# Kernel optimization log

Measured on AMD Instinct MI355X. Metric: run time of the kernel, lower is better.

Reference implementation:

```python
import jax, jax.numpy as jnp
import numpy as np

NEG = -1e6

def setup_inputs() -> dict:
    key = jax.random.key(0)
    ks = jax.random.split(key, 7)
    B, Q, K, H, Dv = 16, 64, 1024, 256, 256
    return {
        "queries": jax.random.normal(ks[0], (B, Q, H), jnp.float32),
        "keys": jax.random.normal(ks[1], (B, K, H), jnp.float32),
        "values": jax.random.normal(ks[2], (B, K, Dv), jnp.float32),
        "valid_lens": jax.random.randint(ks[3], (B,), 1, K + 1),
        "Wq": jax.random.normal(ks[4], (H, H), jnp.float32) / np.sqrt(H),
        "Wk": jax.random.normal(ks[5], (H, H), jnp.float32) / np.sqrt(H),
        "wv": jax.random.normal(ks[6], (H,), jnp.float32) / np.sqrt(H),
    }

def reference(queries, keys, values, valid_lens, Wq, Wk, wv):
    # projections: [B,Q,H], [B,K,H]
    q = jnp.einsum("bqd,hd->bqh", queries, Wq)
    k = jnp.einsum("bkd,hd->bkh", keys, Wk)
    # broadcast add + tanh: [B,Q,K,H]
    features = jnp.tanh(q[:, :, None, :] + k[:, None, :, :])
    # score reduction over hidden: [B,Q,K]
    scores = jnp.einsum("bqkh,h->bqk", features, wv)
    # masked softmax over the key axis (1D valid_lens per batch)
    K = keys.shape[1]
    mask = jnp.arange(K)[None, None, :] < valid_lens[:, None, None]  # [B,1,K]
    scores = jnp.where(mask, scores, NEG)
    attn = jax.nn.softmax(scores, axis=-1)
    # weighted sum over values: [B,Q,Dv]
    return jnp.einsum("bqk,bkv->bqv", attn, values)
```

## Files before the change

### kernel.cpp

```cpp
#include <hip/hip_runtime.h>

#define LOG2E 1.4426950408889634f
#define TANH_SCALE 2.8853900817779268f
#define NEG_BIG -1e30f

typedef __attribute__((ext_vector_type(8))) short bf16x8;
typedef __attribute__((ext_vector_type(4))) float f32x4;
typedef _Float16 half4 __attribute__((ext_vector_type(4)));

static __device__ __forceinline__ short f2bf(float f) {
    unsigned u = __builtin_bit_cast(unsigned, f);
    u += 0x7fffu + ((u >> 16) & 1u);
    return (short)(u >> 16);
}

__global__ __launch_bounds__(256) void proj_mfma(const float* __restrict__ queries,
                                                 const float* __restrict__ keys,
                                                 const float* __restrict__ Wq,
                                                 const float* __restrict__ Wk,
                                                 float* __restrict__ eq,
                                                 float* __restrict__ ek4) {
    const int mt = blockIdx.x >> 1, nt = blockIdx.x & 1;
    const int tid = threadIdx.x;
    const int w = tid >> 6, lane = tid & 63;
    const int wm = w >> 1, wn = w & 1;
    const int r = lane & 15, kq = lane >> 4;
    const int m0 = mt << 5;
    const int ncol = (nt << 7) + (wn << 6);

    const float* A; const float* W; int ar;
    if (m0 < 1024) { A = queries; W = Wq; ar = m0; }
    else           { A = keys;    W = Wk; ar = m0 - 1024; }

    const float* aptr = &A[(size_t)(ar + (wm << 4) + r) * 256];
    f32x4 acc[4] = {};

    #pragma unroll 2
    for (int ks = 0; ks < 8; ++ks) {
        const int k0 = (ks << 5) + (kq << 3);
        float4 fa0 = *reinterpret_cast<const float4*>(aptr + k0);
        float4 fa1 = *reinterpret_cast<const float4*>(aptr + k0 + 4);
        bf16x8 a = {f2bf(fa0.x), f2bf(fa0.y), f2bf(fa0.z), f2bf(fa0.w),
                    f2bf(fa1.x), f2bf(fa1.y), f2bf(fa1.z), f2bf(fa1.w)};
        #pragma unroll
        for (int nj = 0; nj < 4; ++nj) {
            const float* bp = &W[(size_t)(ncol + (nj << 4) + r) * 256 + k0];
            float4 fb0 = *reinterpret_cast<const float4*>(bp);
            float4 fb1 = *reinterpret_cast<const float4*>(bp + 4);
            bf16x8 bb = {f2bf(fb0.x), f2bf(fb0.y), f2bf(fb0.z), f2bf(fb0.w),
                         f2bf(fb1.x), f2bf(fb1.y), f2bf(fb1.z), f2bf(fb1.w)};
            acc[nj] = __builtin_amdgcn_mfma_f32_16x16x32_bf16(a, bb, acc[nj], 0, 0, 0);
        }
    }
    if (m0 < 1024) {
        #pragma unroll
        for (int nj = 0; nj < 4; ++nj)
            #pragma unroll
            for (int t = 0; t < 4; ++t) {
                int row = m0 + (wm << 4) + (kq << 2) + t;
                int col = ncol + (nj << 4) + r;
                eq[(size_t)row * 256 + col] =
                    __builtin_amdgcn_exp2f(TANH_SCALE * acc[nj][t]);
            }
    } else {
        #pragma unroll
        for (int nj = 0; nj < 4; ++nj)
            #pragma unroll
            for (int t = 0; t < 4; ++t) {
                int R   = (m0 - 1024) + (wm << 4) + (kq << 2) + t;
                int col = ncol + (nj << 4) + r;
                size_t idx = ((size_t)((col >> 2) << 14) + R) * 4 + (col & 3);
                ek4[idx] = __builtin_amdgcn_exp2f(TANH_SCALE * acc[nj][t]);
            }
    }
}

__global__ __launch_bounds__(256, 4) void attn_kernel(const float* __restrict__ eq,
                                                      const float* __restrict__ ek4,
                                                      const float* __restrict__ values,
                                                      const int* __restrict__ valid_lens,
                                                      const float* __restrict__ wv,
                                                      _Float16* __restrict__ part_acc,
                                                      float* __restrict__ part_m,
                                                      float* __restrict__ part_l) {
    __shared__ float4 q_lds[8 * 64];
    __shared__ float4 wv_lds[64];
    __shared__ float  p_lds[8][64];

    const int tid = threadIdx.x;
    const int w = tid >> 6, lane = tid & 63;

    const unsigned u = blockIdx.x;
    const int xcd = u & 7;
    const int j   = u >> 3;
    const int qt  = j & 7;
    const int pair = ((j >> 3) << 3) | xcd;
    const int b = pair & 15, seg = pair >> 4;

    const int q0 = qt << 3;
    const int vl = valid_lens[b];
    const int kstart = seg << 7;
    const int pA = (((b << 6) + q0 + (w << 1)) << 3) + seg;
    const int pB = pA + 8;

    if (kstart >= vl) {
        half4 z = {};
        *reinterpret_cast<half4*>(&part_acc[(size_t)pA * 256 + (lane << 2)]) = z;
        *reinterpret_cast<half4*>(&part_acc[(size_t)pB * 256 + (lane << 2)]) = z;
        if (lane == 0) {
            part_m[pA] = NEG_BIG; part_l[pA] = 0.f;
            part_m[pB] = NEG_BIG; part_l[pB] = 0.f;
        }
        return;
    }

    const float4* eqf = reinterpret_cast<const float4*>(eq);
    #pragma unroll
    for (int it = 0; it < 2; ++it) {
        int idx = tid + (it << 8);
        q_lds[idx] = eqf[(size_t)((b << 6) + q0 + (idx >> 6)) * 64 + (idx & 63)];
    }
    if (tid < 64) wv_lds[tid] = *(reinterpret_cast<const float4*>(wv) + tid);
    __syncthreads();

    const int kend = min(kstart + 128, vl);
    const int nchunks = (kend - kstart + 63) >> 6;

    const float4* ek4f = reinterpret_cast<const float4*>(ek4);
    const float4* qa4 = &q_lds[(w << 1) << 6];
    const float4* qb4 = qa4 + 64;

    float mA = -INFINITY, lA = 0.f, mB = -INFINITY, lB = 0.f;
    f32x4 accA = {0.f, 0.f, 0.f, 0.f}, accB = {0.f, 0.f, 0.f, 0.f};

    for (int c = 0; c < nchunks; ++c) {
        const int ck = kstart + (c << 6);
        const float4* ekc = ek4f + (size_t)((b << 10) + ck + lane);

        float sa0 = 0.f, sa1 = 0.f, sa2 = 0.f, sa3 = 0.f;
        float sb0 = 0.f, sb1 = 0.f, sb2 = 0.f, sb3 = 0.f;
        #pragma unroll 8
        for (int h4 = 0; h4 < 64; ++h4) {
            float4 ev = ekc[h4 << 14];
            float4 qa = qa4[h4];
            float4 qb = qb4[h4];
            float4 wc = wv_lds[h4];
            sa0 += wc.x * __builtin_amdgcn_rcpf(fmaf(ev.x, qa.x, 1.0f));
            sa1 += wc.y * __builtin_amdgcn_rcpf(fmaf(ev.y, qa.y, 1.0f));
            sa2 += wc.z * __builtin_amdgcn_rcpf(fmaf(ev.z, qa.z, 1.0f));
            sa3 += wc.w * __builtin_amdgcn_rcpf(fmaf(ev.w, qa.w, 1.0f));
            sb0 += wc.x * __builtin_amdgcn_rcpf(fmaf(ev.x, qb.x, 1.0f));
            sb1 += wc.y * __builtin_amdgcn_rcpf(fmaf(ev.y, qb.y, 1.0f));
            sb2 += wc.z * __builtin_amdgcn_rcpf(fmaf(ev.z, qb.z, 1.0f));
            sb3 += wc.w * __builtin_amdgcn_rcpf(fmaf(ev.w, qb.w, 1.0f));
        }
        float sA_ = -2.0f * ((sa0 + sa1) + (sa2 + sa3));
        float sB_ = -2.0f * ((sb0 + sb1) + (sb2 + sb3));
        if (ck + lane >= vl) { sA_ = NEG_BIG; sB_ = NEG_BIG; }

        float mcA = sA_, mcB = sB_;
        #pragma unroll
        for (int o = 32; o > 0; o >>= 1) {
            mcA = fmaxf(mcA, __shfl_xor(mcA, o));
            mcB = fmaxf(mcB, __shfl_xor(mcB, o));
        }
        float mnA = fmaxf(mA, mcA), mnB = fmaxf(mB, mcB);
        float rA = __builtin_amdgcn_exp2f((mA - mnA) * LOG2E);
        float rB = __builtin_amdgcn_exp2f((mB - mnB) * LOG2E);
        float pA_ = __builtin_amdgcn_exp2f((sA_ - mnA) * LOG2E);
        float pB_ = __builtin_amdgcn_exp2f((sB_ - mnB) * LOG2E);
        float lcA = pA_, lcB = pB_;
        #pragma unroll
        for (int o = 32; o > 0; o >>= 1) {
            lcA += __shfl_xor(lcA, o);
            lcB += __shfl_xor(lcB, o);
        }
        lA = lA * rA + lcA; mA = mnA;
        lB = lB * rB + lcB; mB = mnB;
        accA *= rA; accB *= rB;
        p_lds[(w << 1) + 0][lane] = pA_;
        p_lds[(w << 1) + 1][lane] = pB_;

        const int nv = min(64, kend - ck);
        const float* vsrc = &values[(size_t)(b * 1024 + ck) * 256 + (lane << 2)];
        if (nv == 64) {
            #pragma unroll 4
            for (int j4 = 0; j4 < 16; ++j4) {
                float4 pa4 = *reinterpret_cast<const float4*>(&p_lds[(w << 1)][j4 << 2]);
                float4 pb4 = *reinterpret_cast<const float4*>(&p_lds[(w << 1) + 1][j4 << 2]);
                #pragma unroll
                for (int jj = 0; jj < 4; ++jj) {
                    float pa = ((const float*)&pa4)[jj], pb = ((const float*)&pb4)[jj];
                    float4 v = *reinterpret_cast<const float4*>(vsrc + (((j4 << 2) + jj)) * 256);
                    accA.x += pa * v.x; accA.y += pa * v.y; accA.z += pa * v.z; accA.w += pa * v.w;
                    accB.x += pb * v.x; accB.y += pb * v.y; accB.z += pb * v.z; accB.w += pb * v.w;
                }
            }
        } else {
            for (int jx = 0; jx < nv; ++jx) {
                float pa = p_lds[(w << 1)][jx], pb = p_lds[(w << 1) + 1][jx];
                float4 v = *reinterpret_cast<const float4*>(vsrc + jx * 256);
                accA.x += pa * v.x; accA.y += pa * v.y; accA.z += pa * v.z; accA.w += pa * v.w;
                accB.x += pb * v.x; accB.y += pb * v.y; accB.z += pb * v.z; accB.w += pb * v.w;
            }
        }
    }

    if (lane == 0) {
        part_m[pA] = mA; part_l[pA] = lA;
        part_m[pB] = mB; part_l[pB] = lB;
    }
    half4 ha = {(_Float16)accA.x, (_Float16)accA.y, (_Float16)accA.z, (_Float16)accA.w};
    half4 hb = {(_Float16)accB.x, (_Float16)accB.y, (_Float16)accB.z, (_Float16)accB.w};
    *reinterpret_cast<half4*>(&part_acc[(size_t)pA * 256 + (lane << 2)]) = ha;
    *reinterpret_cast<half4*>(&part_acc[(size_t)pB * 256 + (lane << 2)]) = hb;
}

__global__ __launch_bounds__(256) void combine_kernel(const _Float16* __restrict__ part_acc,
                                                      const float* __restrict__ part_m,
                                                      const float* __restrict__ part_l,
                                                      float* __restrict__ out) {
    const int tid = threadIdx.x;
    const int w = tid >> 6, lane = tid & 63;
    const int b = blockIdx.x >> 4, qt = blockIdx.x & 15;
    const int q = (qt << 2) + w;
    const int base = ((b << 6) + q) << 3;

    float mm[8], ll[8];
    #pragma unroll
    for (int i = 0; i < 8; ++i) { mm[i] = part_m[base + i]; ll[i] = part_l[base + i]; }
    float M = mm[0];
    #pragma unroll
    for (int i = 1; i < 8; ++i) M = fmaxf(M, mm[i]);
    float wt[8];
    float L = 0.f;
    #pragma unroll
    for (int i = 0; i < 8; ++i) {
        wt[i] = __builtin_amdgcn_exp2f((mm[i] - M) * LOG2E);
        L += wt[i] * ll[i];
    }
    float invL = 1.0f / L;
    float4 o = {0.f, 0.f, 0.f, 0.f};
    #pragma unroll
    for (int i = 0; i < 8; ++i) {
        half4 v = *reinterpret_cast<const half4*>(&part_acc[(size_t)(base + i) * 256 + (lane << 2)]);
        o.x += wt[i] * (float)v.x; o.y += wt[i] * (float)v.y;
        o.z += wt[i] * (float)v.z; o.w += wt[i] * (float)v.w;
    }
    o.x *= invL; o.y *= invL; o.z *= invL; o.w *= invL;
    *reinterpret_cast<float4*>(&out[(size_t)((b << 6) + q) * 256 + (lane << 2)]) = o;
}

extern "C" void kernel_launch(void* const* d_in, const int* in_sizes, int n_in,
                              void* d_out, int out_size, void* d_ws, size_t ws_size,
                              hipStream_t stream) {
    const float* queries    = (const float*)d_in[0];
    const float* keys       = (const float*)d_in[1];
    const float* values     = (const float*)d_in[2];
    const int*   valid_lens = (const int*)d_in[3];
    const float* Wq         = (const float*)d_in[4];
    const float* Wk         = (const float*)d_in[5];
    const float* wv         = (const float*)d_in[6];
    float* out = (float*)d_out;

    float*     eq       = (float*)d_ws;
    float*     ek4      = eq + 262144;
    _Float16*  part_acc = (_Float16*)(ek4 + 4194304);
    float*     part_m   = (float*)(part_acc + 2097152);
    float*     part_l   = part_m + 8192;

    proj_mfma<<<dim3(1088), 256, 0, stream>>>(queries, keys, Wq, Wk, eq, ek4);
    attn_kernel<<<dim3(1024), 256, 0, stream>>>(eq, ek4, values, valid_lens, wv,
                                                part_acc, part_m, part_l);
    combine_kernel<<<dim3(256), 256, 0, stream>>>(part_acc, part_m, part_l, out);
}
```

Before: 193.4 us.

## Restructure attention: each wave scores 8 queries over its own 64-key chunk

```diff
diff --git a/kernel.cpp b/kernel.cpp
--- a/kernel.cpp
+++ b/kernel.cpp
@@ -20,6 +20,8 @@
                                                  const float* __restrict__ Wk,
                                                  float* __restrict__ eq,
                                                  float* __restrict__ ek4) {
+    __shared__ float lds_t[128][33];
+
     const int mt = blockIdx.x >> 1, nt = blockIdx.x & 1;
     const int tid = threadIdx.x;
     const int w = tid >> 6, lane = tid & 63;
@@ -67,11 +69,22 @@
         for (int nj = 0; nj < 4; ++nj)
             #pragma unroll
             for (int t = 0; t < 4; ++t) {
-                int R   = (m0 - 1024) + (wm << 4) + (kq << 2) + t;
-                int col = ncol + (nj << 4) + r;
-                size_t idx = ((size_t)((col >> 2) << 14) + R) * 4 + (col & 3);
-                ek4[idx] = __builtin_amdgcn_exp2f(TANH_SCALE * acc[nj][t]);
+                int rloc = (wm << 4) + (kq << 2) + t;
+                int hloc = (wn << 6) + (nj << 4) + r;
+                lds_t[hloc][rloc] = __builtin_amdgcn_exp2f(TANH_SCALE * acc[nj][t]);
             }
+        __syncthreads();
+        const int g0 = nt << 5;
+        const int R0 = m0 - 1024;
+        float4* ek4f = reinterpret_cast<float4*>(ek4);
+        #pragma unroll
+        for (int it = 0; it < 4; ++it) {
+            int idx = (it << 8) + tid;
+            int gl = idx >> 5, kk = idx & 31;
+            float4 v = {lds_t[(gl << 2) + 0][kk], lds_t[(gl << 2) + 1][kk],
+                        lds_t[(gl << 2) + 2][kk], lds_t[(gl << 2) + 3][kk]};
+            ek4f[((size_t)(g0 + gl) << 14) + R0 + kk] = v;
+        }
     }
 }
 
@@ -85,135 +98,97 @@
                                                       float* __restrict__ part_l) {
     __shared__ float4 q_lds[8 * 64];
     __shared__ float4 wv_lds[64];
-    __shared__ float  p_lds[8][64];
+    __shared__ float  p_lds[4][8][64];
 
     const int tid = threadIdx.x;
     const int w = tid >> 6, lane = tid & 63;
-
-    const unsigned u = blockIdx.x;
-    const int xcd = u & 7;
-    const int j   = u >> 3;
-    const int qt  = j & 7;
-    const int pair = ((j >> 3) << 3) | xcd;
-    const int b = pair & 15, seg = pair >> 4;
-
-    const int q0 = qt << 3;
+    const int qoct = blockIdx.x, b = blockIdx.y, seg = blockIdx.z;
+    const int q0 = qoct << 3;
     const int vl = valid_lens[b];
-    const int kstart = seg << 7;
-    const int pA = (((b << 6) + q0 + (w << 1)) << 3) + seg;
-    const int pB = pA + 8;
+    const int cidx = (seg << 2) + w;
+    const int kstart = cidx << 6;
+
+    const float4* eqf = reinterpret_cast<const float4*>(eq);
+    q_lds[tid]       = eqf[(size_t)((b << 6) + q0 + (tid >> 6)) * 64 + (tid & 63)];
+    q_lds[tid + 256] = eqf[(size_t)((b << 6) + q0 + (tid >> 6) + 4) * 64 + (tid & 63)];
+    if (tid < 64) wv_lds[tid] = reinterpret_cast<const float4*>(wv)[tid];
+    __syncthreads();
+
+    const int pbase = ((b << 6) + q0) << 4;
 
     if (kstart >= vl) {
         half4 z = {};
-        *reinterpret_cast<half4*>(&part_acc[(size_t)pA * 256 + (lane << 2)]) = z;
-        *reinterpret_cast<half4*>(&part_acc[(size_t)pB * 256 + (lane << 2)]) = z;
+        #pragma unroll
+        for (int qq = 0; qq < 8; ++qq)
+            *reinterpret_cast<half4*>(
+                &part_acc[(size_t)(pbase + (qq << 4) + cidx) * 256 + (lane << 2)]) = z;
+        if (lane < 8) {
+            part_m[pbase + (lane << 4) + cidx] = NEG_BIG;
+            part_l[pbase + (lane << 4) + cidx] = 0.f;
+        }
+        return;
+    }
+
+    float s[8] = {};
+    const float4* ekc = reinterpret_cast<const float4*>(ek4) + ((b << 10) + kstart + lane);
+    for (int hb = 0; hb < 8; ++hb) {
+        float4 evr[8];
+        #pragma unroll
+        for (int i = 0; i < 8; ++i)
+            evr[i] = ekc[(size_t)((hb << 3) + i) << 14];
+        #pragma unroll
+        for (int i = 0; i < 8; ++i) {
+            const int h4 = (hb << 3) + i;
+            const float4 wc = wv_lds[h4];
+            #pragma unroll
+            for (int qq = 0; qq < 8; ++qq) {
+                const float4 qv = q_lds[(qq << 6) + h4];
+                s[qq] += wc.x * __builtin_amdgcn_rcpf(fmaf(evr[i].x, qv.x, 1.0f))
+                       + wc.y * __builtin_amdgcn_rcpf(fmaf(evr[i].y, qv.y, 1.0f))
+                       + wc.z * __builtin_amdgcn_rcpf(fmaf(evr[i].z, qv.z, 1.0f))
+                       + wc.w * __builtin_amdgcn_rcpf(fmaf(evr[i].w, qv.w, 1.0f));
+            }
+        }
+    }
+
+    const bool valid = (kstart + lane) < vl;
+    #pragma unroll
+    for (int qq = 0; qq < 8; ++qq) {
+        float sc = valid ? (-2.0f * s[qq]) : NEG_BIG;
+        float mx = sc;
+        #pragma unroll
+        for (int o = 32; o > 0; o >>= 1) mx = fmaxf(mx, __shfl_xor(mx, o));
+        float p = __builtin_amdgcn_exp2f((sc - mx) * LOG2E);
+        float ls = p;
+        #pragma unroll
+        for (int o = 32; o > 0; o >>= 1) ls += __shfl_xor(ls, o);
+        p_lds[w][qq][lane] = p;
         if (lane == 0) {
-            part_m[pA] = NEG_BIG; part_l[pA] = 0.f;
-            part_m[pB] = NEG_BIG; part_l[pB] = 0.f;
-        }
-        return;
-    }
-
-    const float4* eqf = reinterpret_cast<const float4*>(eq);
-    #pragma unroll
-    for (int it = 0; it < 2; ++it) {
-        int idx = tid + (it << 8);
-        q_lds[idx] = eqf[(size_t)((b << 6) + q0 + (idx >> 6)) * 64 + (idx & 63)];
-    }
-    if (tid < 64) wv_lds[tid] = *(reinterpret_cast<const float4*>(wv) + tid);
-    __syncthreads();
-
-    const int kend = min(kstart + 128, vl);
-    const int nchunks = (kend - kstart + 63) >> 6;
-
-    const float4* ek4f = reinterpret_cast<const float4*>(ek4);
-    const float4* qa4 = &q_lds[(w << 1) << 6];
-    const float4* qb4 = qa4 + 64;
-
-    float mA = -INFINITY, lA = 0.f, mB = -INFINITY, lB = 0.f;
-    f32x4 accA = {0.f, 0.f, 0.f, 0.f}, accB = {0.f, 0.f, 0.f, 0.f};
-
-    for (int c = 0; c < nchunks; ++c) {
-        const int ck = kstart + (c << 6);
-        const float4* ekc = ek4f + (size_t)((b << 10) + ck + lane);
-
-        float sa0 = 0.f, sa1 = 0.f, sa2 = 0.f, sa3 = 0.f;
-        float sb0 = 0.f, sb1 = 0.f, sb2 = 0.f, sb3 = 0.f;
-        #pragma unroll 8
-        for (int h4 = 0; h4 < 64; ++h4) {
-            float4 ev = ekc[h4 << 14];
-            float4 qa = qa4[h4];
-            float4 qb = qb4[h4];
-            float4 wc = wv_lds[h4];
-            sa0 += wc.x * __builtin_amdgcn_rcpf(fmaf(ev.x, qa.x, 1.0f));
-            sa1 += wc.y * __builtin_amdgcn_rcpf(fmaf(ev.y, qa.y, 1.0f));
-            sa2 += wc.z * __builtin_amdgcn_rcpf(fmaf(ev.z, qa.z, 1.0f));
-            sa3 += wc.w * __builtin_amdgcn_rcpf(fmaf(ev.w, qa.w, 1.0f));
-            sb0 += wc.x * __builtin_amdgcn_rcpf(fmaf(ev.x, qb.x, 1.0f));
-            sb1 += wc.y * __builtin_amdgcn_rcpf(fmaf(ev.y, qb.y, 1.0f));
-            sb2 += wc.z * __builtin_amdgcn_rcpf(fmaf(ev.z, qb.z, 1.0f));
-            sb3 += wc.w * __builtin_amdgcn_rcpf(fmaf(ev.w, qb.w, 1.0f));
-        }
-        float sA_ = -2.0f * ((sa0 + sa1) + (sa2 + sa3));
-        float sB_ = -2.0f * ((sb0 + sb1) + (sb2 + sb3));
-        if (ck + lane >= vl) { sA_ = NEG_BIG; sB_ = NEG_BIG; }
-
-        float mcA = sA_, mcB = sB_;
-        #pragma unroll
-        for (int o = 32; o > 0; o >>= 1) {
-            mcA = fmaxf(mcA, __shfl_xor(mcA, o));
-            mcB = fmaxf(mcB, __shfl_xor(mcB, o));
-        }
-        float mnA = fmaxf(mA, mcA), mnB = fmaxf(mB, mcB);
-        float rA = __builtin_amdgcn_exp2f((mA - mnA) * LOG2E);
-        float rB = __builtin_amdgcn_exp2f((mB - mnB) * LOG2E);
-        float pA_ = __builtin_amdgcn_exp2f((sA_ - mnA) * LOG2E);
-        float pB_ = __builtin_amdgcn_exp2f((sB_ - mnB) * LOG2E);
-        float lcA = pA_, lcB = pB_;
-        #pragma unroll
-        for (int o = 32; o > 0; o >>= 1) {
-            lcA += __shfl_xor(lcA, o);
-            lcB += __shfl_xor(lcB, o);
-        }
-        lA = lA * rA + lcA; mA = mnA;
-        lB = lB * rB + lcB; mB = mnB;
-        accA *= rA; accB *= rB;
-        p_lds[(w << 1) + 0][lane] = pA_;
-        p_lds[(w << 1) + 1][lane] = pB_;
-
-        const int nv = min(64, kend - ck);
-        const float* vsrc = &values[(size_t)(b * 1024 + ck) * 256 + (lane << 2)];
-        if (nv == 64) {
-            #pragma unroll 4
-            for (int j4 = 0; j4 < 16; ++j4) {
-                float4 pa4 = *reinterpret_cast<const float4*>(&p_lds[(w << 1)][j4 << 2]);
-                float4 pb4 = *reinterpret_cast<const float4*>(&p_lds[(w << 1) + 1][j4 << 2]);
-                #pragma unroll
-                for (int jj = 0; jj < 4; ++jj) {
-                    float pa = ((const float*)&pa4)[jj], pb = ((const float*)&pb4)[jj];
-                    float4 v = *reinterpret_cast<const float4*>(vsrc + (((j4 << 2) + jj)) * 256);
-                    accA.x += pa * v.x; accA.y += pa * v.y; accA.z += pa * v.z; accA.w += pa * v.w;
-                    accB.x += pb * v.x; accB.y += pb * v.y; accB.z += pb * v.z; accB.w += pb * v.w;
-                }
-            }
-        } else {
-            for (int jx = 0; jx < nv; ++jx) {
-                float pa = p_lds[(w << 1)][jx], pb = p_lds[(w << 1) + 1][jx];
-                float4 v = *reinterpret_cast<const float4*>(vsrc + jx * 256);
-                accA.x += pa * v.x; accA.y += pa * v.y; accA.z += pa * v.z; accA.w += pa * v.w;
-                accB.x += pb * v.x; accB.y += pb * v.y; accB.z += pb * v.z; accB.w += pb * v.w;
-            }
-        }
-    }
-
-    if (lane == 0) {
-        part_m[pA] = mA; part_l[pA] = lA;
-        part_m[pB] = mB; part_l[pB] = lB;
-    }
-    half4 ha = {(_Float16)accA.x, (_Float16)accA.y, (_Float16)accA.z, (_Float16)accA.w};
-    half4 hb = {(_Float16)accB.x, (_Float16)accB.y, (_Float16)accB.z, (_Float16)accB.w};
-    *reinterpret_cast<half4*>(&part_acc[(size_t)pA * 256 + (lane << 2)]) = ha;
-    *reinterpret_cast<half4*>(&part_acc[(size_t)pB * 256 + (lane << 2)]) = hb;
+            part_m[pbase + (qq << 4) + cidx] = mx;
+            part_l[pbase + (qq << 4) + cidx] = ls;
+        }
+    }
+
+    f32x4 acc[8] = {};
+    const float* vsrc = &values[(size_t)((b << 10) + kstart) * 256 + (lane << 2)];
+    #pragma unroll 4
+    for (int j = 0; j < 64; ++j) {
+        float4 v = *reinterpret_cast<const float4*>(vsrc + j * 256);
+        #pragma unroll
+        for (int qq = 0; qq < 8; ++qq) {
+            float p = p_lds[w][qq][j];
+            acc[qq].x += p * v.x; acc[qq].y += p * v.y;
+            acc[qq].z += p * v.z; acc[qq].w += p * v.w;
+        }
+    }
+
+    #pragma unroll
+    for (int qq = 0; qq < 8; ++qq) {
+        half4 h = {(_Float16)acc[qq].x, (_Float16)acc[qq].y,
+                   (_Float16)acc[qq].z, (_Float16)acc[qq].w};
+        *reinterpret_cast<half4*>(
+            &part_acc[(size_t)(pbase + (qq << 4) + cidx) * 256 + (lane << 2)]) = h;
+    }
 }
 
 __global__ __launch_bounds__(256) void combine_kernel(const _Float16* __restrict__ part_acc,
@@ -224,26 +199,27 @@
     const int w = tid >> 6, lane = tid & 63;
     const int b = blockIdx.x >> 4, qt = blockIdx.x & 15;
     const int q = (qt << 2) + w;
-    const int base = ((b << 6) + q) << 3;
-
-    float mm[8], ll[8];
-    #pragma unroll
-    for (int i = 0; i < 8; ++i) { mm[i] = part_m[base + i]; ll[i] = part_l[base + i]; }
+    const int base = ((b << 6) + q) << 4;
+
+    float mm[16], ll[16];
+    #pragma unroll
+    for (int i = 0; i < 16; ++i) { mm[i] = part_m[base + i]; ll[i] = part_l[base + i]; }
     float M = mm[0];
     #pragma unroll
-    for (int i = 1; i < 8; ++i) M = fmaxf(M, mm[i]);
-    float wt[8];
+    for (int i = 1; i < 16; ++i) M = fmaxf(M, mm[i]);
+    float wt[16];
     float L = 0.f;
     #pragma unroll
-    for (int i = 0; i < 8; ++i) {
+    for (int i = 0; i < 16; ++i) {
         wt[i] = __builtin_amdgcn_exp2f((mm[i] - M) * LOG2E);
         L += wt[i] * ll[i];
     }
     float invL = 1.0f / L;
     float4 o = {0.f, 0.f, 0.f, 0.f};
     #pragma unroll
-    for (int i = 0; i < 8; ++i) {
-        half4 v = *reinterpret_cast<const half4*>(&part_acc[(size_t)(base + i) * 256 + (lane << 2)]);
+    for (int i = 0; i < 16; ++i) {
+        half4 v = *reinterpret_cast<const half4*>(
+            &part_acc[(size_t)(base + i) * 256 + (lane << 2)]);
         o.x += wt[i] * (float)v.x; o.y += wt[i] * (float)v.y;
         o.z += wt[i] * (float)v.z; o.w += wt[i] * (float)v.w;
     }
@@ -263,14 +239,14 @@
     const float* wv         = (const float*)d_in[6];
     float* out = (float*)d_out;
 
-    float*     eq       = (float*)d_ws;
-    float*     ek4      = eq + 262144;
+    float*     eqw      = (float*)d_ws;
+    float*     ek4      = eqw + 262144;
     _Float16*  part_acc = (_Float16*)(ek4 + 4194304);
-    float*     part_m   = (float*)(part_acc + 2097152);
-    float*     part_l   = part_m + 8192;
-
-    proj_mfma<<<dim3(1088), 256, 0, stream>>>(queries, keys, Wq, Wk, eq, ek4);
-    attn_kernel<<<dim3(1024), 256, 0, stream>>>(eq, ek4, values, valid_lens, wv,
-                                                part_acc, part_m, part_l);
+    float*     part_m   = (float*)(part_acc + 4194304);
+    float*     part_l   = part_m + 16384;
+
+    proj_mfma<<<dim3(1088), 256, 0, stream>>>(queries, keys, Wq, Wk, eqw, ek4);
+    attn_kernel<<<dim3(8, 16, 4), 256, 0, stream>>>(eqw, ek4, values, valid_lens, wv,
+                                                    part_acc, part_m, part_l);
     combine_kernel<<<dim3(256), 256, 0, stream>>>(part_acc, part_m, part_l, out);
 }
```

Result: slower. 480.6 us (+148.5%).
